# Kernel tuning notes

Hardware: AMD Instinct MI355X
Metric: run time of the kernel (lower is better)

The kernel has to match this reference:

```python
import jax, jax.numpy as jnp
import numpy as np

B, S, I, F = 2048, 512, 256, 256  # batch, seq_length, input_size, filter_num


def setup_inputs() -> dict:
    key = jax.random.key(0)
    ks = jax.random.split(key, 9)
    sc = 0.05
    return {
        "hidden": jax.random.normal(ks[0], (B, I), jnp.float32),
        "inp": jax.random.normal(ks[1], (B, S, I), jnp.float32),
        "W1": jax.random.normal(ks[2], (F, I), jnp.float32) * sc,   # linear1 weight (no bias)
        "Wc": jax.random.normal(ks[3], (F, S), jnp.float32) * sc,   # conv kernel [F,1,S,1] squeezed
        "bc": jax.random.normal(ks[4], (F,), jnp.float32) * sc,     # conv bias
        "W2": jax.random.normal(ks[5], (I, I + F), jnp.float32) * sc,
        "b2": jax.random.normal(ks[6], (I,), jnp.float32) * sc,
        "Wfc": jax.random.normal(ks[7], (1, I), jnp.float32) * sc,
        "bfc": jax.random.normal(ks[8], (1,), jnp.float32) * sc,
    }


def reference(hidden, inp, W1, Wc, bc, W2, b2, Wfc, bfc):
    # w = linear1(hidden).unsqueeze(1): [B,1,F]
    w = hidden @ W1.T  # [B,F]
    # Conv2d(1,F,kernel=(S,1)) over input [B,1,S,I] -> [B,F,1,I]; kernel spans full
    # time axis with width 1, so it's a contraction over t per input channel i.
    Hc_raw = jnp.einsum('bti,ft->bfi', inp, Wc) + bc[None, :, None]  # [B,F,I]
    # faithful to torch: .squeeze().reshape([-1, input_size, filter_num])
    H_c = Hc_raw.reshape(-1, I, F)  # [B,I,F]
    s = jnp.sum(H_c * w[:, None, :], axis=2)          # [B,I]
    a = jax.nn.sigmoid(s)
    v = jnp.sum(a[:, :, None] * H_c, axis=1)          # [B,F]
    concat = jnp.concatenate([hidden, v], axis=1)     # [B,I+F]
    h_prime = concat @ W2.T + b2                      # [B,I]
    out = h_prime @ Wfc.T + bfc                       # [B,1]
    return out
```

## Files before the change

### kernel.cpp

```cpp
#include <hip/hip_runtime.h>

#define B_ 2048
#define S_ 512
#define I_ 256
#define F_ 256

#define OFF_R    0
#define OFF_C0   512
#define OFF_RS   513
#define OFF_W    1024
#define OFF_SW   (OFF_W + B_*F_)
#define OFF_U    (OFF_SW + B_)
#define OFF_P    (OFF_U + B_*S_)

__global__ __launch_bounds__(256) void k_pre(
    const float* __restrict__ hidden, const float* __restrict__ W1,
    const float* __restrict__ W2, const float* __restrict__ b2,
    const float* __restrict__ Wfc, const float* __restrict__ bfc,
    float* __restrict__ ws) {
  __shared__ float h[4][I_];
  __shared__ float red[256];
  const int tid = threadIdx.x;

  if (blockIdx.x == B_ / 4) {
    const int j = tid;
    float acc0 = 0.f, acc1 = 0.f;
#pragma unroll 8
    for (int i = 0; i < I_; ++i) {
      const float f = Wfc[i];
      acc0 += f * W2[(size_t)i * (I_ + F_) + j];
      acc1 += f * W2[(size_t)i * (I_ + F_) + j + 256];
    }
    ws[OFF_R + j] = acc0;
    ws[OFF_R + 256 + j] = acc1;

    red[j] = Wfc[j] * b2[j];
    __syncthreads();
    for (int s = 128; s > 0; s >>= 1) { if (j < s) red[j] += red[j + s]; __syncthreads(); }
    if (j == 0) ws[OFF_C0] = red[0] + bfc[0];
    __syncthreads();
    red[j] = acc1;
    __syncthreads();
    for (int s = 128; s > 0; s >>= 1) { if (j < s) red[j] += red[j + s]; __syncthreads(); }
    if (j == 0) ws[OFF_RS] = red[0];
    return;
  }

  const int b0 = blockIdx.x * 4;
#pragma unroll
  for (int k = 0; k < 4; ++k) h[k][tid] = hidden[(size_t)(b0 + k) * I_ + tid];
  __syncthreads();

  const int f = tid;
  const float4* wrow = (const float4*)(W1 + (size_t)f * I_);
  float acc[4] = {0.f, 0.f, 0.f, 0.f};
#pragma unroll 4
  for (int iq = 0; iq < I_ / 4; ++iq) {
    const float4 v = wrow[iq];
    const int i = 4 * iq;
#pragma unroll
    for (int k = 0; k < 4; ++k)
      acc[k] += v.x * h[k][i] + v.y * h[k][i + 1] + v.z * h[k][i + 2] + v.w * h[k][i + 3];
  }
#pragma unroll
  for (int k = 0; k < 4; ++k) ws[OFF_W + (size_t)(b0 + k) * F_ + f] = acc[k];

#pragma unroll
  for (int k = 0; k < 4; ++k) {
    red[tid] = acc[k];
    __syncthreads();
    for (int s = 128; s > 0; s >>= 1) { if (tid < s) red[tid] += red[tid + s]; __syncthreads(); }
    if (tid == 0) ws[OFF_SW + b0 + k] = red[0];
    __syncthreads();
  }
}

__global__ __launch_bounds__(256) void k1_scan(
    const float* __restrict__ inp, float* __restrict__ ws) {
  const int b = blockIdx.y;
  const int t0 = blockIdx.x * 64;
  const int lane = threadIdx.x & 63;
  const int wid = threadIdx.x >> 6;
  const int c = lane & 15;
  const int rg = lane >> 4;

  float4 w4[4], rv4[4];
  const float4* wptr = (const float4*)(ws + OFF_W + (size_t)b * F_);
  const float4* rvptr = (const float4*)(ws + OFF_R + 256);
#pragma unroll
  for (int j = 0; j < 4; ++j) { w4[j] = wptr[c * 4 + j]; rv4[j] = rvptr[c * 4 + j]; }

  const float* base = inp + ((size_t)b * S_ + t0) * I_;
  float* uo = ws + OFF_U + (size_t)b * S_ + t0;
  float* po = ws + OFF_P + (size_t)b * S_ + t0;

#pragma unroll
  for (int g = 0; g < 4; ++g) {
    const int row = wid * 16 + g * 4 + rg;
    const float4* rbase = (const float4*)(base + (size_t)row * I_ + c * 16);
    float du = 0.f, dp = 0.f;
#pragma unroll
    for (int j = 0; j < 4; ++j) {
      const float4 v = rbase[j];
      du += v.x * w4[j].x + v.y * w4[j].y + v.z * w4[j].z + v.w * w4[j].w;
      dp += v.x * rv4[j].x + v.y * rv4[j].y + v.z * rv4[j].z + v.w * rv4[j].w;
    }
#pragma unroll
    for (int m = 8; m >= 1; m >>= 1) {
      du += __shfl_xor(du, m, 64);
      dp += __shfl_xor(dp, m, 64);
    }
    if (c == 0) { uo[row] = du; po[row] = dp; }
  }
}

__global__ __launch_bounds__(256) void k2_epilogue(
    const float* __restrict__ Wc, const float* __restrict__ bc,
    const float* __restrict__ hidden, const float* __restrict__ ws,
    float* __restrict__ out) {
  const int b0 = blockIdx.x * 4;
  const int tid = threadIdx.x;
  const int lane = tid & 63;
  const int wid = tid >> 6;
  __shared__ float u[4][S_];
  __shared__ float p[4][S_];
  __shared__ float wred[4][4];
  const float* wsu = ws + OFF_U;
  const float* wsp = ws + OFF_P;
#pragma unroll
  for (int k = 0; k < 4; ++k) {
    u[k][tid]       = wsu[(size_t)(b0 + k) * S_ + tid];
    u[k][tid + 256] = wsu[(size_t)(b0 + k) * S_ + tid + 256];
    p[k][tid]       = wsp[(size_t)(b0 + k) * S_ + tid];
    p[k][tid + 256] = wsp[(size_t)(b0 + k) * S_ + tid + 256];
  }
  __syncthreads();

  const int x = tid;
  const float4* wrow = (const float4*)(Wc + (size_t)x * S_);
  float ss[4] = {0.f, 0.f, 0.f, 0.f};
  float qs[4] = {0.f, 0.f, 0.f, 0.f};
#pragma unroll 4
  for (int tq = 0; tq < S_ / 4; ++tq) {
    const float4 v = wrow[tq];
    const int t = 4 * tq;
#pragma unroll
    for (int k = 0; k < 4; ++k) {
      ss[k] += v.x * u[k][t] + v.y * u[k][t + 1] + v.z * u[k][t + 2] + v.w * u[k][t + 3];
      qs[k] += v.x * p[k][t] + v.y * p[k][t + 1] + v.z * p[k][t + 2] + v.w * p[k][t + 3];
    }
  }

  const float bcx = bc[x];
  const float R = ws[OFF_RS];
  const float rh = ws[OFF_R + x];
  const float c0 = ws[OFF_C0];

#pragma unroll
  for (int k = 0; k < 4; ++k) {
    const float Sw = ws[OFF_SW + b0 + k];
    const float s = ss[k] + bcx * Sw;
    const float a = 1.f / (1.f + expf(-s));
    float partial = a * (qs[k] + bcx * R) + rh * hidden[(size_t)(b0 + k) * I_ + x];
#pragma unroll
    for (int m = 32; m >= 1; m >>= 1) partial += __shfl_xor(partial, m, 64);
    if (lane == 0) wred[k][wid] = partial;
  }
  __syncthreads();
  if (tid < 4)
    out[b0 + tid] = wred[tid][0] + wred[tid][1] + wred[tid][2] + wred[tid][3] + c0;
}

extern "C" void kernel_launch(void* const* d_in, const int* in_sizes, int n_in,
                              void* d_out, int out_size, void* d_ws, size_t ws_size,
                              hipStream_t stream) {
  (void)in_sizes; (void)n_in; (void)out_size; (void)ws_size;
  const float* hidden = (const float*)d_in[0];
  const float* inp    = (const float*)d_in[1];
  const float* W1     = (const float*)d_in[2];
  const float* Wc     = (const float*)d_in[3];
  const float* bc     = (const float*)d_in[4];
  const float* W2     = (const float*)d_in[5];
  const float* b2     = (const float*)d_in[6];
  const float* Wfc    = (const float*)d_in[7];
  const float* bfc    = (const float*)d_in[8];
  float* out = (float*)d_out;
  float* ws  = (float*)d_ws;

  hipLaunchKernelGGL(k_pre, dim3(B_ / 4 + 1), dim3(256), 0, stream,
                     hidden, W1, W2, b2, Wfc, bfc, ws);
  hipLaunchKernelGGL(k1_scan, dim3(S_ / 64, B_), dim3(256), 0, stream, inp, ws);
  hipLaunchKernelGGL(k2_epilogue, dim3(B_ / 4), dim3(256), 0, stream, Wc, bc, hidden, ws, out);
}
```

Measured before the change: 287.7 us.

## Split W2 fold across blocks, one block per batch in scan, nontemporal loads

The single serial block that folded Wfc into W2 is split into 8 partial-sum blocks, and the reductions for R and c0 move into the epilogue. The scan kernel now uses one block per batch row, looping over all 512 timesteps with nontemporal loads of the large input tensor. The epilogue reads u/p straight from global memory instead of staging them in shared memory. This aims to remove the serial tail block from the prologue and cut the streaming cost of the input, at the price of fewer, longer scan blocks and redundant partial-sum reductions in every block.

```diff
diff --git a/kernel.cpp b/kernel.cpp
--- a/kernel.cpp
+++ b/kernel.cpp
@@ -4,48 +4,39 @@
 #define S_ 512
 #define I_ 256
 #define F_ 256
-
-#define OFF_R    0
-#define OFF_C0   512
-#define OFF_RS   513
+#define NG 8
+
+typedef float v4f __attribute__((ext_vector_type(4)));
+
 #define OFF_W    1024
 #define OFF_SW   (OFF_W + B_*F_)
 #define OFF_U    (OFF_SW + B_)
 #define OFF_P    (OFF_U + B_*S_)
+#define OFF_RP   (OFF_P + B_*S_)
 
 __global__ __launch_bounds__(256) void k_pre(
     const float* __restrict__ hidden, const float* __restrict__ W1,
-    const float* __restrict__ W2, const float* __restrict__ b2,
-    const float* __restrict__ Wfc, const float* __restrict__ bfc,
+    const float* __restrict__ W2, const float* __restrict__ Wfc,
     float* __restrict__ ws) {
+  const int tid = threadIdx.x;
+
+  if (blockIdx.x >= B_ / 4) {
+    const int g = blockIdx.x - B_ / 4;
+    float acc0 = 0.f, acc1 = 0.f;
+#pragma unroll 8
+    for (int ii = 0; ii < 32; ++ii) {
+      const int i = g * 32 + ii;
+      const float f = Wfc[i];
+      acc0 += f * W2[(size_t)i * (I_ + F_) + tid];
+      acc1 += f * W2[(size_t)i * (I_ + F_) + tid + 256];
+    }
+    ws[OFF_RP + g * 512 + tid] = acc0;
+    ws[OFF_RP + g * 512 + 256 + tid] = acc1;
+    return;
+  }
+
   __shared__ float h[4][I_];
   __shared__ float red[256];
-  const int tid = threadIdx.x;
-
-  if (blockIdx.x == B_ / 4) {
-    const int j = tid;
-    float acc0 = 0.f, acc1 = 0.f;
-#pragma unroll 8
-    for (int i = 0; i < I_; ++i) {
-      const float f = Wfc[i];
-      acc0 += f * W2[(size_t)i * (I_ + F_) + j];
-      acc1 += f * W2[(size_t)i * (I_ + F_) + j + 256];
-    }
-    ws[OFF_R + j] = acc0;
-    ws[OFF_R + 256 + j] = acc1;
-
-    red[j] = Wfc[j] * b2[j];
-    __syncthreads();
-    for (int s = 128; s > 0; s >>= 1) { if (j < s) red[j] += red[j + s]; __syncthreads(); }
-    if (j == 0) ws[OFF_C0] = red[0] + bfc[0];
-    __syncthreads();
-    red[j] = acc1;
-    __syncthreads();
-    for (int s = 128; s > 0; s >>= 1) { if (j < s) red[j] += red[j + s]; __syncthreads(); }
-    if (j == 0) ws[OFF_RS] = red[0];
-    return;
-  }
-
   const int b0 = blockIdx.x * 4;
 #pragma unroll
   for (int k = 0; k < 4; ++k) h[k][tid] = hidden[(size_t)(b0 + k) * I_ + tid];
@@ -76,34 +67,45 @@
 }
 
 __global__ __launch_bounds__(256) void k1_scan(
-    const float* __restrict__ inp, float* __restrict__ ws) {
-  const int b = blockIdx.y;
-  const int t0 = blockIdx.x * 64;
-  const int lane = threadIdx.x & 63;
-  const int wid = threadIdx.x >> 6;
+    const float* __restrict__ inp, const float* __restrict__ wsw,
+    const float* __restrict__ wsrp,
+    float* __restrict__ wsu, float* __restrict__ wsp) {
+  const int b = blockIdx.x;
+  const int tid = threadIdx.x;
+  __shared__ float sh[512];
+
+  float rv = 0.f;
+#pragma unroll
+  for (int g = 0; g < NG; ++g) rv += wsrp[g * 512 + 256 + tid];
+  sh[256 + tid] = rv;
+  sh[tid] = wsw[(size_t)b * F_ + tid];
+  __syncthreads();
+
+  const int lane = tid & 63;
+  const int wid = tid >> 6;
   const int c = lane & 15;
   const int rg = lane >> 4;
 
   float4 w4[4], rv4[4];
-  const float4* wptr = (const float4*)(ws + OFF_W + (size_t)b * F_);
-  const float4* rvptr = (const float4*)(ws + OFF_R + 256);
-#pragma unroll
-  for (int j = 0; j < 4; ++j) { w4[j] = wptr[c * 4 + j]; rv4[j] = rvptr[c * 4 + j]; }
-
-  const float* base = inp + ((size_t)b * S_ + t0) * I_;
-  float* uo = ws + OFF_U + (size_t)b * S_ + t0;
-  float* po = ws + OFF_P + (size_t)b * S_ + t0;
-
-#pragma unroll
-  for (int g = 0; g < 4; ++g) {
-    const int row = wid * 16 + g * 4 + rg;
-    const float4* rbase = (const float4*)(base + (size_t)row * I_ + c * 16);
+#pragma unroll
+  for (int j = 0; j < 4; ++j) {
+    w4[j]  = ((const float4*)sh)[c * 4 + j];
+    rv4[j] = ((const float4*)(sh + 256))[c * 4 + j];
+  }
+
+  const float* base = inp + (size_t)b * S_ * I_;
+  float* uo = wsu + (size_t)b * S_;
+  float* po = wsp + (size_t)b * S_;
+
+  for (int gg = 0; gg < 32; ++gg) {
+    const int row = gg * 16 + wid * 4 + rg;
+    const v4f* rbase = (const v4f*)(base + (size_t)row * I_ + c * 16);
     float du = 0.f, dp = 0.f;
 #pragma unroll
     for (int j = 0; j < 4; ++j) {
-      const float4 v = rbase[j];
-      du += v.x * w4[j].x + v.y * w4[j].y + v.z * w4[j].z + v.w * w4[j].w;
-      dp += v.x * rv4[j].x + v.y * rv4[j].y + v.z * rv4[j].z + v.w * rv4[j].w;
+      const v4f v = __builtin_nontemporal_load(rbase + j);
+      du += v[0] * w4[j].x + v[1] * w4[j].y + v[2] * w4[j].z + v[3] * w4[j].w;
+      dp += v[0] * rv4[j].x + v[1] * rv4[j].y + v[2] * rv4[j].z + v[3] * rv4[j].w;
     }
 #pragma unroll
     for (int m = 8; m >= 1; m >>= 1) {
@@ -116,49 +118,54 @@
 
 __global__ __launch_bounds__(256) void k2_epilogue(
     const float* __restrict__ Wc, const float* __restrict__ bc,
-    const float* __restrict__ hidden, const float* __restrict__ ws,
+    const float* __restrict__ b2, const float* __restrict__ Wfc,
+    const float* __restrict__ bfc, const float* __restrict__ hidden,
+    const float* __restrict__ wsu, const float* __restrict__ wsp,
+    const float* __restrict__ wsSw, const float* __restrict__ wsrp,
     float* __restrict__ out) {
   const int b0 = blockIdx.x * 4;
-  const int tid = threadIdx.x;
-  const int lane = tid & 63;
-  const int wid = tid >> 6;
-  __shared__ float u[4][S_];
-  __shared__ float p[4][S_];
+  const int x = threadIdx.x;
+  const int lane = x & 63;
+  const int wid = x >> 6;
+  __shared__ float shred[2][4];
   __shared__ float wred[4][4];
-  const float* wsu = ws + OFF_U;
-  const float* wsp = ws + OFF_P;
-#pragma unroll
-  for (int k = 0; k < 4; ++k) {
-    u[k][tid]       = wsu[(size_t)(b0 + k) * S_ + tid];
-    u[k][tid + 256] = wsu[(size_t)(b0 + k) * S_ + tid + 256];
-    p[k][tid]       = wsp[(size_t)(b0 + k) * S_ + tid];
-    p[k][tid + 256] = wsp[(size_t)(b0 + k) * S_ + tid + 256];
-  }
-  __syncthreads();
-
-  const int x = tid;
+
+  float rh = 0.f, rv = 0.f;
+#pragma unroll
+  for (int g = 0; g < NG; ++g) {
+    rh += wsrp[g * 512 + x];
+    rv += wsrp[g * 512 + 256 + x];
+  }
+  float t0 = rv, t1 = Wfc[x] * b2[x];
+#pragma unroll
+  for (int m = 32; m >= 1; m >>= 1) {
+    t0 += __shfl_xor(t0, m, 64);
+    t1 += __shfl_xor(t1, m, 64);
+  }
+  if (lane == 0) { shred[0][wid] = t0; shred[1][wid] = t1; }
+  __syncthreads();
+  const float R  = shred[0][0] + shred[0][1] + shred[0][2] + shred[0][3];
+  const float c0 = shred[1][0] + shred[1][1] + shred[1][2] + shred[1][3] + bfc[0];
+
   const float4* wrow = (const float4*)(Wc + (size_t)x * S_);
   float ss[4] = {0.f, 0.f, 0.f, 0.f};
   float qs[4] = {0.f, 0.f, 0.f, 0.f};
-#pragma unroll 4
   for (int tq = 0; tq < S_ / 4; ++tq) {
     const float4 v = wrow[tq];
     const int t = 4 * tq;
 #pragma unroll
     for (int k = 0; k < 4; ++k) {
-      ss[k] += v.x * u[k][t] + v.y * u[k][t + 1] + v.z * u[k][t + 2] + v.w * u[k][t + 3];
-      qs[k] += v.x * p[k][t] + v.y * p[k][t + 1] + v.z * p[k][t + 2] + v.w * p[k][t + 3];
+      const float4 u4 = *(const float4*)(wsu + (size_t)(b0 + k) * S_ + t);
+      const float4 p4 = *(const float4*)(wsp + (size_t)(b0 + k) * S_ + t);
+      ss[k] += v.x * u4.x + v.y * u4.y + v.z * u4.z + v.w * u4.w;
+      qs[k] += v.x * p4.x + v.y * p4.y + v.z * p4.z + v.w * p4.w;
     }
   }
 
   const float bcx = bc[x];
-  const float R = ws[OFF_RS];
-  const float rh = ws[OFF_R + x];
-  const float c0 = ws[OFF_C0];
-
 #pragma unroll
   for (int k = 0; k < 4; ++k) {
-    const float Sw = ws[OFF_SW + b0 + k];
+    const float Sw = wsSw[b0 + k];
     const float s = ss[k] + bcx * Sw;
     const float a = 1.f / (1.f + expf(-s));
     float partial = a * (qs[k] + bcx * R) + rh * hidden[(size_t)(b0 + k) * I_ + x];
@@ -167,8 +174,8 @@
     if (lane == 0) wred[k][wid] = partial;
   }
   __syncthreads();
-  if (tid < 4)
-    out[b0 + tid] = wred[tid][0] + wred[tid][1] + wred[tid][2] + wred[tid][3] + c0;
+  if (x < 4)
+    out[b0 + x] = wred[x][0] + wred[x][1] + wred[x][2] + wred[x][3] + c0;
 }
 
 extern "C" void kernel_launch(void* const* d_in, const int* in_sizes, int n_in,
@@ -187,8 +194,11 @@
   float* out = (float*)d_out;
   float* ws  = (float*)d_ws;
 
-  hipLaunchKernelGGL(k_pre, dim3(B_ / 4 + 1), dim3(256), 0, stream,
-                     hidden, W1, W2, b2, Wfc, bfc, ws);
-  hipLaunchKernelGGL(k1_scan, dim3(S_ / 64, B_), dim3(256), 0, stream, inp, ws);
-  hipLaunchKernelGGL(k2_epilogue, dim3(B_ / 4), dim3(256), 0, stream, Wc, bc, hidden, ws, out);
-}
+  hipLaunchKernelGGL(k_pre, dim3(B_ / 4 + NG), dim3(256), 0, stream,
+                     hidden, W1, W2, Wfc, ws);
+  hipLaunchKernelGGL(k1_scan, dim3(B_), dim3(256), 0, stream,
+                     inp, ws + OFF_W, ws + OFF_RP, ws + OFF_U, ws + OFF_P);
+  hipLaunchKernelGGL(k2_epilogue, dim3(B_ / 4), dim3(256), 0, stream,
+                     Wc, bc, b2, Wfc, bfc, hidden,
+                     ws + OFF_U, ws + OFF_P, ws + OFF_SW, ws + OFF_RP, out);
+}
```

Measured after the change: 359.3 us. 1.25x slower.
